# Optimization experiments

Hardware: AMD Instinct MI355X
Metric: run time of the kernel (lower is better)

## Reference

```python
import jax, jax.numpy as jnp
import numpy as np

OVERFLOW_MARGIN = 1e-08

N, D, OUT = 8192, 128, 128


def setup_inputs() -> dict:
    key = jax.random.key(0)
    k1, k2, k3 = jax.random.split(key, 3)
    values = jax.random.normal(k1, (N, D), dtype=jnp.float32)
    adjacency = jax.random.uniform(k2, (N, N), dtype=jnp.float32)
    W = jax.random.normal(k3, (D, OUT), dtype=jnp.float32) * 0.05
    b = jnp.zeros((OUT,), dtype=jnp.float32)
    return {"values": values, "adjacency": adjacency, "W": W, "b": b}


def reference(values, adjacency, W, b):
    # Dense projection: fc_sc = values @ W + b  -> [N, OUT]
    fc_sc = values @ W + b
    # degree d = A @ ones -> row sums, [N]
    d = jnp.sum(adjacency, axis=1)
    d_inv_sqrt = 1.0 / (jnp.sqrt(d) + OVERFLOW_MARGIN)  # [N]
    # laplacian = diag(d_inv_sqrt) @ A @ diag(d_inv_sqrt)
    # expressed as row/col broadcast scaling (same math, no NxN diag matmuls)
    laplacian = adjacency * d_inv_sqrt[:, None] * d_inv_sqrt[None, :]
    # graph conv: [N,N] @ [N,OUT]
    return laplacian @ fc_sc
```

## Files before the change

### kernel.cpp

```cpp
#include <hip/hip_runtime.h>

#define NROWS 8192
#define DIM   128
#define RS    132
#define PSTR  520

typedef __attribute__((ext_vector_type(8))) short  short8;
typedef __attribute__((ext_vector_type(4))) float  floatx4;

__device__ __forceinline__ unsigned pk_bf16(float a, float b) {
  unsigned ua = __float_as_uint(a);
  ua += 0x7fffu + ((ua >> 16) & 1u);
  unsigned ub = __float_as_uint(b);
  ub += 0x7fffu + ((ub >> 16) & 1u);
  return (ua >> 16) | (ub & 0xffff0000u);
}

__global__ __launch_bounds__(256) void k_prep(const float* __restrict__ A,
                                              float* __restrict__ d,
                                              unsigned short* __restrict__ Abf) {
  __shared__ unsigned short B[16 * PSTR];
  __shared__ float rsum[16 * 17];
  int iblk = blockIdx.x;
  int wb   = blockIdx.y;
  int i0   = iblk * 16;
  int jwin = wb * 512;
  int t = threadIdx.x;
  int r = t >> 4, l16 = t & 15;

  const float* ap = A + (size_t)(i0 + r) * NROWS + jwin + l16 * 8;
  float sum = 0.f;
#pragma unroll
  for (int it = 0; it < 4; ++it) {
    float4 lo = *(const float4*)(ap + it * 128);
    float4 hi = *(const float4*)(ap + it * 128 + 4);
    sum += (lo.x + lo.y) + (lo.z + lo.w) + (hi.x + hi.y) + (hi.z + hi.w);
    uint4 p = make_uint4(pk_bf16(lo.x, lo.y), pk_bf16(lo.z, lo.w),
                         pk_bf16(hi.x, hi.y), pk_bf16(hi.z, hi.w));
    *(uint4*)&B[r * PSTR + l16 * 8 + it * 128] = p;
  }
  rsum[r * 17 + l16] = sum;
  __syncthreads();
  if (t < 16) {
    float s2 = 0.f;
#pragma unroll
    for (int c = 0; c < 16; ++c) s2 += rsum[t * 17 + c];
    atomicAdd(&d[i0 + t], s2);
  }
  int jb = t >> 4, p = t & 15;
  unsigned short* tbase = Abf + ((size_t)iblk * 256 + wb * 16 + jb) * 512;
#pragma unroll
  for (int q = 0; q < 4; ++q) {
    uint4 v = *(const uint4*)&B[p * PSTR + jb * 32 + q * 8];
    *(uint4*)(tbase + (size_t)(q * 16 + p) * 8) = v;
  }
}

__global__ __launch_bounds__(256) void k_sconv(const float* __restrict__ d,
                                               float* __restrict__ s) {
  int i = blockIdx.x * 256 + threadIdx.x;
  s[i] = 1.0f / (sqrtf(d[i]) + 1e-8f);
}

__global__ __launch_bounds__(256) void k_fc(const float* __restrict__ V,
                                            const float* __restrict__ W,
                                            const float* __restrict__ b,
                                            const float* __restrict__ s,
                                            unsigned short* __restrict__ gTt) {
  __shared__ float Wl[DIM * DIM];
  __shared__ float Vl[32 * DIM];
  __shared__ unsigned short Fl[32 * DIM];
  int r0 = blockIdx.x * 32;
  {
    const float4* Wg = (const float4*)W;
    float4* Wd = (float4*)Wl;
#pragma unroll
    for (int i = 0; i < DIM * DIM / 4 / 256; ++i)
      Wd[threadIdx.x + i * 256] = Wg[threadIdx.x + i * 256];
    const float4* Vg = (const float4*)(V + (size_t)r0 * DIM);
    float4* Vd = (float4*)Vl;
#pragma unroll
    for (int i = 0; i < 32 * DIM / 4 / 256; ++i)
      Vd[threadIdx.x + i * 256] = Vg[threadIdx.x + i * 256];
  }
  __syncthreads();

  int cg = threadIdx.x & 31;
  int rg = threadIdx.x >> 5;
  float acc[4][4] = {};
  for (int dd = 0; dd < DIM; ++dd) {
    float4 w = *(const float4*)&Wl[dd * DIM + cg * 4];
#pragma unroll
    for (int rr = 0; rr < 4; ++rr) {
      float v = Vl[(rg * 4 + rr) * DIM + dd];
      acc[rr][0] += v * w.x; acc[rr][1] += v * w.y;
      acc[rr][2] += v * w.z; acc[rr][3] += v * w.w;
    }
  }
  float bb[4], sv[4];
#pragma unroll
  for (int cc = 0; cc < 4; ++cc) bb[cc] = b[cg * 4 + cc];
#pragma unroll
  for (int rr = 0; rr < 4; ++rr) sv[rr] = s[r0 + rg * 4 + rr];
#pragma unroll
  for (int rr = 0; rr < 4; ++rr)
#pragma unroll
    for (int cc = 0; cc < 4; cc += 2) {
      unsigned p = pk_bf16((acc[rr][cc]     + bb[cc])     * sv[rr],
                           (acc[rr][cc + 1] + bb[cc + 1]) * sv[rr]);
      *(unsigned*)&Fl[(rg * 4 + rr) * DIM + cg * 4 + cc] = p;
    }
  __syncthreads();

  int kblk = threadIdx.x >> 5, s5 = threadIdx.x & 31;
  int jblk = r0 >> 5;
#pragma unroll
  for (int h = 0; h < 2; ++h) {
    int L = s5 + h * 32;
    int l15 = L & 15, quad = L >> 4;
    int k = kblk * 16 + l15;
    unsigned w0 = (unsigned)Fl[(quad * 8 + 0) * DIM + k] | ((unsigned)Fl[(quad * 8 + 1) * DIM + k] << 16);
    unsigned w1 = (unsigned)Fl[(quad * 8 + 2) * DIM + k] | ((unsigned)Fl[(quad * 8 + 3) * DIM + k] << 16);
    unsigned w2 = (unsigned)Fl[(quad * 8 + 4) * DIM + k] | ((unsigned)Fl[(quad * 8 + 5) * DIM + k] << 16);
    unsigned w3 = (unsigned)Fl[(quad * 8 + 6) * DIM + k] | ((unsigned)Fl[(quad * 8 + 7) * DIM + k] << 16);
    *(uint4*)(gTt + ((size_t)(kblk * 256 + jblk) * 64 + L) * 8) = make_uint4(w0, w1, w2, w3);
  }
}

__global__ __launch_bounds__(256, 4) void k_spmm(const unsigned short* __restrict__ Abf,
                                                 const unsigned short* __restrict__ gTt,
                                                 const float* __restrict__ s,
                                                 float* __restrict__ out) {
  __shared__ float red[4 * 32 * RS];
  int t = threadIdx.x, w = t >> 6, lane = t & 63;
  int bi = blockIdx.x;
  int jblk0 = w * 64;

  const unsigned short* ab = Abf + ((size_t)bi * 2 * 256 + jblk0) * 512 + lane * 8;
  const unsigned short* gb = gTt + (size_t)jblk0 * 512 + lane * 8;

  floatx4 acc[8][2];
#pragma unroll
  for (int kb = 0; kb < 8; ++kb)
#pragma unroll
    for (int ib = 0; ib < 2; ++ib)
      acc[kb][ib] = (floatx4){0.f, 0.f, 0.f, 0.f};

#pragma unroll 2
  for (int it = 0; it < 64; ++it) {
    short8 af0 = *(const short8*)(ab);
    short8 af1 = *(const short8*)(ab + (size_t)256 * 512);
    short8 gf[8];
#pragma unroll
    for (int kb = 0; kb < 8; ++kb)
      gf[kb] = *(const short8*)(gb + (size_t)kb * 256 * 512);
#pragma unroll
    for (int kb = 0; kb < 8; ++kb) {
      acc[kb][0] = __builtin_amdgcn_mfma_f32_16x16x32_bf16(gf[kb], af0, acc[kb][0], 0, 0, 0);
      acc[kb][1] = __builtin_amdgcn_mfma_f32_16x16x32_bf16(gf[kb], af1, acc[kb][1], 0, 0, 0);
    }
    ab += 512; gb += 512;
  }

  int l15 = lane & 15, quad = lane >> 4;
  float* myred = red + w * 32 * RS;
#pragma unroll
  for (int ib = 0; ib < 2; ++ib)
#pragma unroll
    for (int kb = 0; kb < 8; ++kb) {
      float4 v = make_float4(acc[kb][ib][0], acc[kb][ib][1], acc[kb][ib][2], acc[kb][ib][3]);
      *(float4*)(myred + (ib * 16 + l15) * RS + kb * 16 + quad * 4) = v;
    }
  __syncthreads();

  int ii = t >> 3, kg = (t & 7) * 16;
  float4 sum[4];
#pragma unroll
  for (int c = 0; c < 4; ++c) sum[c] = make_float4(0.f, 0.f, 0.f, 0.f);
#pragma unroll
  for (int ww = 0; ww < 4; ++ww)
#pragma unroll
    for (int c = 0; c < 4; ++c) {
      float4 v = *(const float4*)(red + ww * 32 * RS + ii * RS + kg + c * 4);
      sum[c].x += v.x; sum[c].y += v.y; sum[c].z += v.z; sum[c].w += v.w;
    }
  float si = s[bi * 32 + ii];
  float* pout = out + ((size_t)(bi * 32 + ii)) * 128 + kg;
#pragma unroll
  for (int c = 0; c < 4; ++c) {
    float4 r = make_float4(si * sum[c].x, si * sum[c].y, si * sum[c].z, si * sum[c].w);
    *(float4*)(pout + c * 4) = r;
  }
}

extern "C" void kernel_launch(void* const* d_in, const int* in_sizes, int n_in,
                              void* d_out, int out_size, void* d_ws, size_t ws_size,
                              hipStream_t stream) {
  const float* values    = (const float*)d_in[0];
  const float* adjacency = (const float*)d_in[1];
  const float* W         = (const float*)d_in[2];
  const float* b         = (const float*)d_in[3];
  float* out = (float*)d_out;

  char* ws = (char*)d_ws;
  float* d            = (float*)ws;
  float* s            = (float*)(ws + 32768);
  unsigned short* gTt = (unsigned short*)(ws + 65536);
  unsigned short* Abf = (unsigned short*)(ws + 65536 + 2097152);

  hipMemsetAsync(d, 0, NROWS * sizeof(float), stream);
  k_prep<<<dim3(512, 16), 256, 0, stream>>>(adjacency, d, Abf);
  k_sconv<<<NROWS / 256, 256, 0, stream>>>(d, s);
  k_fc<<<NROWS / 32, 256, 0, stream>>>(values, W, b, s, gTt);
  k_spmm<<<256, 256, 0, stream>>>(Abf, gTt, s, out);
}
```

Before: 477.6 us.

## Drop bf16 adjacency staging and convert fp32 adjacency inside SpMM

The prep kernel that wrote a tiled bf16 copy of the adjacency matrix is removed. A lightweight row-sum kernel now computes the degrees with one wave per row and a shuffle reduction, which also removes the memset and the atomics. The SpMM kernel reads fp32 adjacency rows directly and packs them to bf16 in registers before the MFMA. This avoids writing and re-reading the 128MB intermediate. In exchange the SpMM streams twice as many bytes, in 128-byte row segments that coalesce less well, and its occupancy hint drops from 4 to 2.

```diff
diff --git a/kernel.cpp b/kernel.cpp
--- a/kernel.cpp
+++ b/kernel.cpp
@@ -3,7 +3,6 @@
 #define NROWS 8192
 #define DIM   128
 #define RS    132
-#define PSTR  520
 
 typedef __attribute__((ext_vector_type(8))) short  short8;
 typedef __attribute__((ext_vector_type(4))) float  floatx4;
@@ -16,44 +15,20 @@
   return (ua >> 16) | (ub & 0xffff0000u);
 }
 
-__global__ __launch_bounds__(256) void k_prep(const float* __restrict__ A,
-                                              float* __restrict__ d,
-                                              unsigned short* __restrict__ Abf) {
-  __shared__ unsigned short B[16 * PSTR];
-  __shared__ float rsum[16 * 17];
-  int iblk = blockIdx.x;
-  int wb   = blockIdx.y;
-  int i0   = iblk * 16;
-  int jwin = wb * 512;
-  int t = threadIdx.x;
-  int r = t >> 4, l16 = t & 15;
-
-  const float* ap = A + (size_t)(i0 + r) * NROWS + jwin + l16 * 8;
+__global__ __launch_bounds__(256) void k_rowsum(const float* __restrict__ A,
+                                                float* __restrict__ d) {
+  int w = threadIdx.x >> 6, lane = threadIdx.x & 63;
+  int row = blockIdx.x * 4 + w;
+  const float* ap = A + (size_t)row * NROWS + lane * 4;
   float sum = 0.f;
 #pragma unroll
-  for (int it = 0; it < 4; ++it) {
-    float4 lo = *(const float4*)(ap + it * 128);
-    float4 hi = *(const float4*)(ap + it * 128 + 4);
-    sum += (lo.x + lo.y) + (lo.z + lo.w) + (hi.x + hi.y) + (hi.z + hi.w);
-    uint4 p = make_uint4(pk_bf16(lo.x, lo.y), pk_bf16(lo.z, lo.w),
-                         pk_bf16(hi.x, hi.y), pk_bf16(hi.z, hi.w));
-    *(uint4*)&B[r * PSTR + l16 * 8 + it * 128] = p;
+  for (int it = 0; it < 32; ++it) {
+    float4 v = *(const float4*)(ap + (size_t)it * 256);
+    sum += (v.x + v.y) + (v.z + v.w);
   }
-  rsum[r * 17 + l16] = sum;
-  __syncthreads();
-  if (t < 16) {
-    float s2 = 0.f;
 #pragma unroll
-    for (int c = 0; c < 16; ++c) s2 += rsum[t * 17 + c];
-    atomicAdd(&d[i0 + t], s2);
-  }
-  int jb = t >> 4, p = t & 15;
-  unsigned short* tbase = Abf + ((size_t)iblk * 256 + wb * 16 + jb) * 512;
-#pragma unroll
-  for (int q = 0; q < 4; ++q) {
-    uint4 v = *(const uint4*)&B[p * PSTR + jb * 32 + q * 8];
-    *(uint4*)(tbase + (size_t)(q * 16 + p) * 8) = v;
-  }
+  for (int off = 32; off; off >>= 1) sum += __shfl_down(sum, off, 64);
+  if (lane == 0) d[row] = sum;
 }
 
 __global__ __launch_bounds__(256) void k_sconv(const float* __restrict__ d,
@@ -127,16 +102,18 @@
   }
 }
 
-__global__ __launch_bounds__(256, 4) void k_spmm(const unsigned short* __restrict__ Abf,
+__global__ __launch_bounds__(256, 2) void k_spmm(const float* __restrict__ A,
                                                  const unsigned short* __restrict__ gTt,
                                                  const float* __restrict__ s,
                                                  float* __restrict__ out) {
   __shared__ float red[4 * 32 * RS];
   int t = threadIdx.x, w = t >> 6, lane = t & 63;
+  int l15 = lane & 15, quad = lane >> 4;
   int bi = blockIdx.x;
   int jblk0 = w * 64;
 
-  const unsigned short* ab = Abf + ((size_t)bi * 2 * 256 + jblk0) * 512 + lane * 8;
+  const float* ap0 = A + (size_t)(bi * 32 + l15) * NROWS + jblk0 * 32 + quad * 8;
+  const float* ap1 = ap0 + (size_t)16 * NROWS;
   const unsigned short* gb = gTt + (size_t)jblk0 * 512 + lane * 8;
 
   floatx4 acc[8][2];
@@ -148,21 +125,27 @@
 
 #pragma unroll 2
   for (int it = 0; it < 64; ++it) {
-    short8 af0 = *(const short8*)(ab);
-    short8 af1 = *(const short8*)(ab + (size_t)256 * 512);
+    float4 a0lo = *(const float4*)(ap0);
+    float4 a0hi = *(const float4*)(ap0 + 4);
+    float4 a1lo = *(const float4*)(ap1);
+    float4 a1hi = *(const float4*)(ap1 + 4);
     short8 gf[8];
 #pragma unroll
     for (int kb = 0; kb < 8; ++kb)
       gf[kb] = *(const short8*)(gb + (size_t)kb * 256 * 512);
+    union { unsigned u[4]; short8 s8; } c0, c1;
+    c0.u[0] = pk_bf16(a0lo.x, a0lo.y); c0.u[1] = pk_bf16(a0lo.z, a0lo.w);
+    c0.u[2] = pk_bf16(a0hi.x, a0hi.y); c0.u[3] = pk_bf16(a0hi.z, a0hi.w);
+    c1.u[0] = pk_bf16(a1lo.x, a1lo.y); c1.u[1] = pk_bf16(a1lo.z, a1lo.w);
+    c1.u[2] = pk_bf16(a1hi.x, a1hi.y); c1.u[3] = pk_bf16(a1hi.z, a1hi.w);
 #pragma unroll
     for (int kb = 0; kb < 8; ++kb) {
-      acc[kb][0] = __builtin_amdgcn_mfma_f32_16x16x32_bf16(gf[kb], af0, acc[kb][0], 0, 0, 0);
-      acc[kb][1] = __builtin_amdgcn_mfma_f32_16x16x32_bf16(gf[kb], af1, acc[kb][1], 0, 0, 0);
+      acc[kb][0] = __builtin_amdgcn_mfma_f32_16x16x32_bf16(gf[kb], c0.s8, acc[kb][0], 0, 0, 0);
+      acc[kb][1] = __builtin_amdgcn_mfma_f32_16x16x32_bf16(gf[kb], c1.s8, acc[kb][1], 0, 0, 0);
     }
-    ab += 512; gb += 512;
+    ap0 += 32; ap1 += 32; gb += 512;
   }
 
-  int l15 = lane & 15, quad = lane >> 4;
   float* myred = red + w * 32 * RS;
 #pragma unroll
   for (int ib = 0; ib < 2; ++ib)
@@ -206,11 +189,9 @@
   float* d            = (float*)ws;
   float* s            = (float*)(ws + 32768);
   unsigned short* gTt = (unsigned short*)(ws + 65536);
-  unsigned short* Abf = (unsigned short*)(ws + 65536 + 2097152);
 
-  hipMemsetAsync(d, 0, NROWS * sizeof(float), stream);
-  k_prep<<<dim3(512, 16), 256, 0, stream>>>(adjacency, d, Abf);
+  k_rowsum<<<NROWS / 4, 256, 0, stream>>>(adjacency, d);
   k_sconv<<<NROWS / 256, 256, 0, stream>>>(d, s);
   k_fc<<<NROWS / 32, 256, 0, stream>>>(values, W, b, s, gTt);
-  k_spmm<<<256, 256, 0, stream>>>(Abf, gTt, s, out);
+  k_spmm<<<256, 256, 0, stream>>>(adjacency, gTt, s, out);
 }
```

Result: faster. 431.6 us (-9.6%).
